# Performance work log

Measured on AMD Instinct MI355X. Metric: run time of the kernel, lower is better.

## Reference

```python
import jax, jax.numpy as jnp
import numpy as np

B, T, D = 4, 2048, 512
E, H, K = 8, 512, 2


def setup_inputs() -> dict:
    key = jax.random.key(0)
    ks = jax.random.split(key, 8)
    s_in = 1.0 / np.sqrt(D)
    s_h = 1.0 / np.sqrt(H)
    return {
        "x": jax.random.normal(ks[0], (B, T, D), dtype=jnp.float32),
        "Wg": jax.random.uniform(ks[1], (D, E), jnp.float32, -s_in, s_in),
        "bg": jax.random.uniform(ks[2], (E,), jnp.float32, -s_in, s_in),
        "W1": jax.random.uniform(ks[3], (E, D, H), jnp.float32, -s_in, s_in),
        "b1": jax.random.uniform(ks[4], (E, H), jnp.float32, -s_in, s_in),
        "W2": jax.random.uniform(ks[5], (E, H, H), jnp.float32, -s_h, s_h),
        "b2": jax.random.uniform(ks[6], (E, H), jnp.float32, -s_h, s_h),
    }


def reference(x, Wg, bg, W1, b1, W2, b2):
    Bx, Tx, Dx = x.shape
    xf = x.reshape(-1, Dx)                                   # [N, D]
    # --- gate (noise_std = 0) ---
    logits = xf @ Wg + bg                                    # [N, E]
    topk_scores, topk_idx = jax.lax.top_k(logits, K)         # [N, K]
    topk_w = jax.nn.softmax(topk_scores, axis=-1)            # K=2 -> softmax over selected
    # --- experts: dense compute, then gather the selected ones ---
    h = jax.nn.gelu(jnp.einsum('nd,edh->neh', xf, W1) + b1, approximate=False)  # [N, E, H]
    y = jnp.einsum('neh,ehf->nef', h, W2) + b2               # [N, E, H]
    sel = jnp.take_along_axis(y, topk_idx[:, :, None], axis=1)  # [N, K, H]
    out = jnp.sum(topk_w[:, :, None] * sel, axis=1)          # weighted combine [N, H]
    return out.reshape(Bx, Tx, -1)
```

## Files before the change

kernel.cpp:

```cpp
#include <hip/hip_runtime.h>
#include <hip/hip_bf16.h>


typedef __bf16 bf16x8 __attribute__((ext_vector_type(8)));
typedef float  f32x4  __attribute__((ext_vector_type(4)));

#define N_TOK 8192
#define D_IN  512
#define N_EXP 8
#define H_DIM 512

static __device__ __forceinline__ unsigned short f2bf(float f) {
    union { float f; unsigned u; } v; v.f = f;
    unsigned r = v.u + 0x7FFFu + ((v.u >> 16) & 1u);
    return (unsigned short)(r >> 16);
}
static __device__ __forceinline__ float gelu_exact(float v) {
    return 0.5f * v * (1.0f + erff(v * 0.70710678118654752f));
}
static __device__ __forceinline__ void gload_lds16(const void* src, void* lds_dst) {
    __builtin_amdgcn_global_load_lds(
        (const __attribute__((address_space(1))) unsigned int*)src,
        (__attribute__((address_space(3))) unsigned int*)lds_dst, 16, 0, 0);
}

__global__ void __launch_bounds__(256) k_pack(const float* __restrict__ W1,
                                              const float* __restrict__ W2,
                                              unsigned short* __restrict__ w1f,
                                              unsigned short* __restrict__ w2f) {
    __shared__ float t[32][65];
    int z = blockIdx.z;
    int e = z & 7;
    const float* in = (z < 8) ? W1 : W2;
    unsigned short* out = (z < 8) ? w1f : w2f;
    int cb0 = blockIdx.x * 4;
    int kc  = blockIdx.y;
    const float* src = in + ((size_t)e * 512 + kc * 32) * 512 + blockIdx.x * 64;
    int tid = threadIdx.x;
    int r = tid >> 3, cq = (tid & 7) * 8;
    float4 v0 = *(const float4*)(src + (size_t)r * 512 + cq);
    float4 v1 = *(const float4*)(src + (size_t)r * 512 + cq + 4);
    t[r][cq + 0] = v0.x; t[r][cq + 1] = v0.y; t[r][cq + 2] = v0.z; t[r][cq + 3] = v0.w;
    t[r][cq + 4] = v1.x; t[r][cq + 5] = v1.y; t[r][cq + 6] = v1.z; t[r][cq + 7] = v1.w;
    __syncthreads();
    int g = tid >> 6, lane = tid & 63;
    int l15 = lane & 15, l4 = lane >> 4;
    unsigned v[4];
    #pragma unroll
    for (int j = 0; j < 4; ++j) {
        unsigned lo = f2bf(t[l4 * 8 + 2 * j    ][g * 16 + l15]);
        unsigned hi = f2bf(t[l4 * 8 + 2 * j + 1][g * 16 + l15]);
        v[j] = lo | (hi << 16);
    }
    size_t dst = (((size_t)(e * 32 + cb0 + g) * 16 + kc) * 512) + lane * 8;
    *(uint4*)(out + dst) = make_uint4(v[0], v[1], v[2], v[3]);
}

__global__ void __launch_bounds__(256) k_gate(const float* __restrict__ x,
                                              const float* __restrict__ Wg,
                                              const float* __restrict__ bg,
                                              unsigned char* __restrict__ sel,
                                              float2* __restrict__ w2,
                                              unsigned short* __restrict__ xbf) {
    __shared__ float part[32][8][8];
    __shared__ float lg[32][8];
    int tid = threadIdx.x;
    int t = tid >> 3, c = tid & 7;
    int n0 = blockIdx.x * 32;
    int n = n0 + t;
    const float4* xr = (const float4*)(x + (size_t)n * D_IN + c * 64);
    float acc[8];
    #pragma unroll
    for (int e = 0; e < 8; ++e) acc[e] = 0.f;
    #pragma unroll
    for (int j4 = 0; j4 < 16; ++j4) {
        float4 v = xr[j4];
        int k = c * 64 + j4 * 4;
        float xv[4] = {v.x, v.y, v.z, v.w};
        #pragma unroll
        for (int u = 0; u < 4; ++u) {
            float4 wlo = *(const float4*)(Wg + (size_t)(k + u) * 8);
            float4 whi = *(const float4*)(Wg + (size_t)(k + u) * 8 + 4);
            acc[0] += xv[u] * wlo.x; acc[1] += xv[u] * wlo.y;
            acc[2] += xv[u] * wlo.z; acc[3] += xv[u] * wlo.w;
            acc[4] += xv[u] * whi.x; acc[5] += xv[u] * whi.y;
            acc[6] += xv[u] * whi.z; acc[7] += xv[u] * whi.w;
        }
    }
    #pragma unroll
    for (int e = 0; e < 8; ++e) part[t][c][e] = acc[e];
    __syncthreads();
    {
        float f = bg[c];
        #pragma unroll
        for (int cc = 0; cc < 8; ++cc) f += part[t][cc][c];
        lg[t][c] = f;
    }
    __syncthreads();
    if (c == 0) {
        float best = lg[t][0]; int i1 = 0;
        #pragma unroll
        for (int j = 1; j < 8; ++j) { float v = lg[t][j]; if (v > best) { best = v; i1 = j; } }
        float best2 = -1e30f; int i2 = 0;
        #pragma unroll
        for (int j = 0; j < 8; ++j) {
            if (j == i1) continue;
            float v = lg[t][j]; if (v > best2) { best2 = v; i2 = j; }
        }
        float tt = expf(best2 - best);
        float w0 = 1.0f / (1.0f + tt);
        sel[n] = (unsigned char)(i1 | (i2 << 4));
        w2[n] = make_float2(w0, 1.0f - w0);
    }
    #pragma unroll
    for (int i = 0; i < 8; ++i) {
        int idx = tid + i * 256;
        int r = idx >> 6, g = idx & 63;
        const float* src = x + (size_t)(n0 + r) * D_IN + g * 8;
        float4 a = *(const float4*)src;
        float4 b = *(const float4*)(src + 4);
        unsigned u0 = (unsigned)f2bf(a.x) | ((unsigned)f2bf(a.y) << 16);
        unsigned u1 = (unsigned)f2bf(a.z) | ((unsigned)f2bf(a.w) << 16);
        unsigned u2 = (unsigned)f2bf(b.x) | ((unsigned)f2bf(b.y) << 16);
        unsigned u3 = (unsigned)f2bf(b.z) | ((unsigned)f2bf(b.w) << 16);
        *(uint4*)(xbf + (size_t)(n0 + r) * D_IN + g * 8) = make_uint4(u0, u1, u2, u3);
    }
}

__global__ void __launch_bounds__(1024) k_build(const unsigned char* __restrict__ sel,
                                                const float2* __restrict__ w2,
                                                int* __restrict__ counts,
                                                int* __restrict__ lists,
                                                float* __restrict__ wgts) {
    int e = blockIdx.x;
    __shared__ int tot[8][16];
    __shared__ int cbase[8];
    int tid = threadIdx.x, lane = tid & 63, wv = tid >> 6;
    unsigned long long masks[8];
    unsigned char svals[8];
    #pragma unroll
    for (int c = 0; c < 8; ++c) {
        int n = c * 1024 + tid;
        unsigned char s = sel[n];
        svals[c] = s;
        bool f = ((s & 15) == e) || ((s >> 4) == e);
        masks[c] = __ballot(f);
        if (lane == 0) tot[c][wv] = __popcll(masks[c]);
    }
    __syncthreads();
    if (tid == 0) {
        int b = 0;
        #pragma unroll
        for (int c = 0; c < 8; ++c) {
            cbase[c] = b;
            #pragma unroll
            for (int i = 0; i < 16; ++i) b += tot[c][i];
        }
        counts[e] = b;
    }
    __syncthreads();
    #pragma unroll
    for (int c = 0; c < 8; ++c) {
        if ((masks[c] >> lane) & 1ull) {
            int wb = cbase[c];
            for (int i = 0; i < wv; ++i) wb += tot[c][i];
            int pos = wb + __popcll(masks[c] & ((1ull << lane) - 1ull));
            int n = c * 1024 + tid;
            bool f1 = ((svals[c] & 15) == e);
            lists[e * N_TOK + pos] = (n << 1) | (f1 ? 0 : 1);
            float2 w = w2[n];
            wgts[e * N_TOK + pos] = f1 ? w.x : w.y;
        }
    }
}

__global__ void __launch_bounds__(512, 4)
k_l1(const unsigned short* __restrict__ xbf,
     const unsigned short* __restrict__ w1f, const float* __restrict__ b1,
     const int* __restrict__ counts, const int* __restrict__ lists,
     unsigned short* __restrict__ hbuf) {
    __shared__ unsigned short lds[64 * D_IN];
    __shared__ int tl[64];

    int b = blockIdx.x;
    int e = b & 7;
    int rest = b >> 3;
    int tile = rest >> 1, ch = rest & 1;
    int cnt = counts[e];
    int row0 = tile * 64;
    if (row0 >= cnt) return;
    int rv = min(64, cnt - row0);
    int gb = row0;
    #pragma unroll
    for (int i = 0; i < 8; ++i) gb += (i < e) ? ((counts[i] + 63) & ~63) : 0;

    int tid = threadIdx.x, lane = tid & 63, wid = tid >> 6;
    int l15 = lane & 15, l4 = lane >> 4;
    if (tid < 64) tl[tid] = (tid < rv) ? lists[e * N_TOK + row0 + tid] : 0;

    const unsigned short* wbase = w1f + ((size_t)(e * 32 + ch * 16 + wid * 2) * 16) * 512 + (size_t)lane * 8;
    bf16x8 bb[4][2];
    #pragma unroll
    for (int n = 0; n < 2; ++n) {
        bb[0][n] = *(const bf16x8*)(wbase + (n * 16 + 0) * 512);
        bb[1][n] = *(const bf16x8*)(wbase + (n * 16 + 1) * 512);
        bb[2][n] = *(const bf16x8*)(wbase + (n * 16 + 2) * 512);
    }
    float bv[2];
    #pragma unroll
    for (int n = 0; n < 2; ++n) bv[n] = b1[e * H_DIM + ch * 256 + wid * 32 + n * 16 + l15];
    __syncthreads();

    #pragma unroll
    for (int i = 0; i < 8; ++i) {
        int row = wid * 8 + i;
        if (row < rv) {
            int tok = tl[row] >> 1;
            const char* src = (const char*)xbf + ((size_t)tok << 10)
                            + ((lane * 16) ^ ((row & 7) << 4));
            gload_lds16(src, (char*)lds + row * 1024);
        } else {
            *(uint4*)((char*)lds + row * 1024 + lane * 16) = make_uint4(0, 0, 0, 0);
        }
    }
    __syncthreads();

    f32x4 acc[4][2];
    #pragma unroll
    for (int n = 0; n < 2; ++n)
        #pragma unroll
        for (int m = 0; m < 4; ++m) acc[m][n] = f32x4{bv[n], bv[n], bv[n], bv[n]};

    #pragma unroll
    for (int kc = 0; kc < 16; ++kc) {
        if (kc + 3 < 16) {
            #pragma unroll
            for (int n = 0; n < 2; ++n)
                bb[(kc + 3) & 3][n] = *(const bf16x8*)(wbase + (n * 16 + kc + 3) * 512);
        }
        int k0 = kc * 32 + l4 * 8;
        bf16x8 a[4];
        #pragma unroll
        for (int m = 0; m < 4; ++m) {
            int row = m * 16 + l15;
            int off = (row * 1024 + k0 * 2) ^ ((row & 7) << 4);
            a[m] = *(const bf16x8*)((const char*)lds + off);
        }
        #pragma unroll
        for (int n = 0; n < 2; ++n)
            #pragma unroll
            for (int m = 0; m < 4; ++m)
                acc[m][n] = __builtin_amdgcn_mfma_f32_16x16x32_bf16(a[m], bb[kc & 3][n], acc[m][n], 0, 0, 0);
    }
    __syncthreads();

    #pragma unroll
    for (int m = 0; m < 4; ++m)
        #pragma unroll
        for (int n = 0; n < 2; ++n)
            #pragma unroll
            for (int r = 0; r < 4; ++r) {
                int row = m * 16 + l4 * 4 + r;
                int lcol = wid * 32 + n * 16 + l15;
                lds[row * 256 + lcol] = f2bf(gelu_exact(acc[m][n][r]));
            }
    __syncthreads();
    #pragma unroll
    for (int it = 0; it < 4; ++it) {
        int idx = tid + it * 512;
        int row = idx >> 5, g = idx & 31;
        if (row < rv)
            *(uint4*)(hbuf + (size_t)(gb + row) * 512 + ch * 256 + g * 8) =
                *(uint4*)(lds + row * 256 + g * 8);
    }
}

__global__ void __launch_bounds__(512, 4)
k_l2(const unsigned short* __restrict__ hbuf,
     const unsigned short* __restrict__ w2f, const float* __restrict__ b2,
     const int* __restrict__ counts, const int* __restrict__ lists,
     const float* __restrict__ wgts, float* __restrict__ out) {
    __shared__ unsigned short lds[64 * D_IN];
    __shared__ int   tl[64];
    __shared__ float wl[64];

    int b = blockIdx.x;
    int e = b & 7;
    int rest = b >> 3;
    int tile = rest >> 1, ch = rest & 1;
    int cnt = counts[e];
    int row0 = tile * 64;
    if (row0 >= cnt) return;
    int rv = min(64, cnt - row0);
    int gb = row0;
    #pragma unroll
    for (int i = 0; i < 8; ++i) gb += (i < e) ? ((counts[i] + 63) & ~63) : 0;

    int tid = threadIdx.x, lane = tid & 63, wid = tid >> 6;
    int l15 = lane & 15, l4 = lane >> 4;
    if (tid < 64) {
        int v = 0; float w = 0.f;
        if (tid < rv) {
            v = lists[e * N_TOK + row0 + tid];
            w = wgts [e * N_TOK + row0 + tid];
        }
        tl[tid] = v; wl[tid] = w;
    }

    const unsigned short* wbase = w2f + ((size_t)(e * 32 + ch * 16 + wid * 2) * 16) * 512 + (size_t)lane * 8;
    bf16x8 bb[4][2];
    #pragma unroll
    for (int n = 0; n < 2; ++n) {
        bb[0][n] = *(const bf16x8*)(wbase + (n * 16 + 0) * 512);
        bb[1][n] = *(const bf16x8*)(wbase + (n * 16 + 1) * 512);
        bb[2][n] = *(const bf16x8*)(wbase + (n * 16 + 2) * 512);
    }
    float bv[2];
    #pragma unroll
    for (int n = 0; n < 2; ++n) bv[n] = b2[e * H_DIM + ch * 256 + wid * 32 + n * 16 + l15];
    __syncthreads();

    #pragma unroll
    for (int i = 0; i < 8; ++i) {
        int row = wid * 8 + i;
        if (row < rv) {
            const char* src = (const char*)hbuf + (((size_t)(gb + row)) << 10)
                            + ((lane * 16) ^ ((row & 7) << 4));
            gload_lds16(src, (char*)lds + row * 1024);
        } else {
            *(uint4*)((char*)lds + row * 1024 + lane * 16) = make_uint4(0, 0, 0, 0);
        }
    }
    __syncthreads();

    f32x4 acc[4][2];
    #pragma unroll
    for (int n = 0; n < 2; ++n)
        #pragma unroll
        for (int m = 0; m < 4; ++m) acc[m][n] = f32x4{bv[n], bv[n], bv[n], bv[n]};

    #pragma unroll
    for (int kc = 0; kc < 16; ++kc) {
        if (kc + 3 < 16) {
            #pragma unroll
            for (int n = 0; n < 2; ++n)
                bb[(kc + 3) & 3][n] = *(const bf16x8*)(wbase + (n * 16 + kc + 3) * 512);
        }
        int k0 = kc * 32 + l4 * 8;
        bf16x8 a[4];
        #pragma unroll
        for (int m = 0; m < 4; ++m) {
            int row = m * 16 + l15;
            int off = (row * 1024 + k0 * 2) ^ ((row & 7) << 4);
            a[m] = *(const bf16x8*)((const char*)lds + off);
        }
        #pragma unroll
        for (int n = 0; n < 2; ++n)
            #pragma unroll
            for (int m = 0; m < 4; ++m)
                acc[m][n] = __builtin_amdgcn_mfma_f32_16x16x32_bf16(a[m], bb[kc & 3][n], acc[m][n], 0, 0, 0);
    }

    #pragma unroll
    for (int m = 0; m < 4; ++m)
        #pragma unroll
        for (int r = 0; r < 4; ++r) {
            int row = m * 16 + l4 * 4 + r;
            if (row < rv) {
                int t = tl[row] >> 1;
                float gw = wl[row];
                #pragma unroll
                for (int n = 0; n < 2; ++n) {
                    int col = ch * 256 + wid * 32 + n * 16 + l15;
                    atomicAdd(out + (size_t)t * H_DIM + col, gw * acc[m][n][r]);
                }
            }
        }
}

extern "C" void kernel_launch(void* const* d_in, const int* in_sizes, int n_in,
                              void* d_out, int out_size, void* d_ws, size_t ws_size,
                              hipStream_t stream) {
    (void)in_sizes; (void)n_in; (void)ws_size;
    const float* x  = (const float*)d_in[0];
    const float* Wg = (const float*)d_in[1];
    const float* bg = (const float*)d_in[2];
    const float* W1 = (const float*)d_in[3];
    const float* b1 = (const float*)d_in[4];
    const float* W2 = (const float*)d_in[5];
    const float* b2 = (const float*)d_in[6];
    float* out = (float*)d_out;

    char* ws = (char*)d_ws;
    unsigned short* w1f = (unsigned short*)(ws);
    unsigned short* w2f = (unsigned short*)(ws + (4ull << 20));
    unsigned short* hbuf= (unsigned short*)(ws + (8ull << 20));
    unsigned short* xbf = (unsigned short*)(ws + (25ull << 20));
    char* tail = ws + (33ull << 20);
    int*   counts = (int*)(tail);
    int*   lists  = (int*)(tail + 256);
    float* wgts   = (float*)(tail + 256 + 262144);
    unsigned char* sel = (unsigned char*)(tail + 256 + 524288);
    float2* w2g   = (float2*)(tail + 256 + 532480);

    hipMemsetAsync(out, 0, (size_t)out_size * sizeof(float), stream);

    k_pack<<<dim3(8, 16, 16), dim3(256), 0, stream>>>(W1, W2, w1f, w2f);
    k_gate<<<dim3(N_TOK / 32), dim3(256), 0, stream>>>(x, Wg, bg, sel, w2g, xbf);
    k_build<<<dim3(N_EXP), dim3(1024), 0, stream>>>(sel, w2g, counts, lists, wgts);
    k_l1<<<dim3(2048), dim3(512), 0, stream>>>(xbf, w1f, b1, counts, lists, hbuf);
    k_l2<<<dim3(2048), dim3(512), 0, stream>>>(hbuf, w2f, b2, counts, lists, wgts, out);
}
```

Baseline: 181.8 us.

## Replace atomic scatter-add combine with bf16 slot buffer and separate combine kernel

The second-layer kernel no longer atomically adds weighted results into the output. It stages each gate-weighted tile in LDS as bf16 and writes it with coalesced stores into a per-(token, slot) buffer. A new combine kernel sums the two slots per token into fp32 output, which also removes the output memset. This trades scattered fp32 atomics for an extra kernel launch and round trip through memory, and it rounds each expert's contribution to bf16 before the sum.

```diff
diff --git a/kernel.cpp b/kernel.cpp
--- a/kernel.cpp
+++ b/kernel.cpp
@@ -14,6 +14,9 @@
     union { float f; unsigned u; } v; v.f = f;
     unsigned r = v.u + 0x7FFFu + ((v.u >> 16) & 1u);
     return (unsigned short)(r >> 16);
+}
+static __device__ __forceinline__ float bf2f(unsigned short h) {
+    union { unsigned u; float f; } v; v.u = ((unsigned)h) << 16; return v.f;
 }
 static __device__ __forceinline__ float gelu_exact(float v) {
     return 0.5f * v * (1.0f + erff(v * 0.70710678118654752f));
@@ -279,7 +282,8 @@
 k_l2(const unsigned short* __restrict__ hbuf,
      const unsigned short* __restrict__ w2f, const float* __restrict__ b2,
      const int* __restrict__ counts, const int* __restrict__ lists,
-     const float* __restrict__ wgts, float* __restrict__ out) {
+     const float* __restrict__ wgts,
+     unsigned short* __restrict__ ybuf) {
     __shared__ unsigned short lds[64 * D_IN];
     __shared__ int   tl[64];
     __shared__ float wl[64];
@@ -361,27 +365,52 @@
                 acc[m][n] = __builtin_amdgcn_mfma_f32_16x16x32_bf16(a[m], bb[kc & 3][n], acc[m][n], 0, 0, 0);
     }
 
+    __syncthreads();
     #pragma unroll
     for (int m = 0; m < 4; ++m)
         #pragma unroll
-        for (int r = 0; r < 4; ++r) {
-            int row = m * 16 + l4 * 4 + r;
-            if (row < rv) {
-                int t = tl[row] >> 1;
-                float gw = wl[row];
-                #pragma unroll
-                for (int n = 0; n < 2; ++n) {
-                    int col = ch * 256 + wid * 32 + n * 16 + l15;
-                    atomicAdd(out + (size_t)t * H_DIM + col, gw * acc[m][n][r]);
-                }
+        for (int n = 0; n < 2; ++n)
+            #pragma unroll
+            for (int r = 0; r < 4; ++r) {
+                int row = m * 16 + l4 * 4 + r;
+                int lcol = wid * 32 + n * 16 + l15;
+                lds[row * 256 + lcol] = f2bf(acc[m][n][r] * wl[row]);
             }
-        }
+    __syncthreads();
+    #pragma unroll
+    for (int it = 0; it < 4; ++it) {
+        int idx = tid + it * 512;
+        int row = idx >> 5, g = idx & 31;
+        if (row < rv)
+            *(uint4*)(ybuf + (size_t)tl[row] * 512 + ch * 256 + g * 8) =
+                *(uint4*)(lds + row * 256 + g * 8);
+    }
+}
+
+__global__ void __launch_bounds__(256) k_combine(const unsigned short* __restrict__ yb,
+                                                 float* __restrict__ out) {
+    int gid = blockIdx.x * 256 + threadIdx.x;
+    int n = gid >> 6;
+    int h0 = (gid & 63) * 8;
+    const unsigned short* r0 = yb + ((size_t)2 * n) * H_DIM + h0;
+    uint4 a = *(const uint4*)r0;
+    uint4 b = *(const uint4*)(r0 + H_DIM);
+    float o[8];
+    unsigned ua[4] = {a.x, a.y, a.z, a.w}, ub[4] = {b.x, b.y, b.z, b.w};
+    #pragma unroll
+    for (int j = 0; j < 4; ++j) {
+        o[2 * j]     = bf2f((unsigned short)(ua[j] & 0xFFFF)) + bf2f((unsigned short)(ub[j] & 0xFFFF));
+        o[2 * j + 1] = bf2f((unsigned short)(ua[j] >> 16))    + bf2f((unsigned short)(ub[j] >> 16));
+    }
+    float* dst = out + (size_t)n * H_DIM + h0;
+    *(float4*)dst       = make_float4(o[0], o[1], o[2], o[3]);
+    *(float4*)(dst + 4) = make_float4(o[4], o[5], o[6], o[7]);
 }
 
 extern "C" void kernel_launch(void* const* d_in, const int* in_sizes, int n_in,
                               void* d_out, int out_size, void* d_ws, size_t ws_size,
                               hipStream_t stream) {
-    (void)in_sizes; (void)n_in; (void)ws_size;
+    (void)in_sizes; (void)n_in; (void)ws_size; (void)out_size;
     const float* x  = (const float*)d_in[0];
     const float* Wg = (const float*)d_in[1];
     const float* bg = (const float*)d_in[2];
@@ -394,20 +423,20 @@
     char* ws = (char*)d_ws;
     unsigned short* w1f = (unsigned short*)(ws);
     unsigned short* w2f = (unsigned short*)(ws + (4ull << 20));
-    unsigned short* hbuf= (unsigned short*)(ws + (8ull << 20));
-    unsigned short* xbf = (unsigned short*)(ws + (25ull << 20));
-    char* tail = ws + (33ull << 20);
+    unsigned short* ybuf= (unsigned short*)(ws + (8ull << 20));
+    unsigned short* hbuf= (unsigned short*)(ws + (24ull << 20));
+    unsigned short* xbf = (unsigned short*)(ws + (41ull << 20));
+    char* tail = ws + (49ull << 20);
     int*   counts = (int*)(tail);
     int*   lists  = (int*)(tail + 256);
     float* wgts   = (float*)(tail + 256 + 262144);
     unsigned char* sel = (unsigned char*)(tail + 256 + 524288);
     float2* w2g   = (float2*)(tail + 256 + 532480);
 
-    hipMemsetAsync(out, 0, (size_t)out_size * sizeof(float), stream);
-
     k_pack<<<dim3(8, 16, 16), dim3(256), 0, stream>>>(W1, W2, w1f, w2f);
     k_gate<<<dim3(N_TOK / 32), dim3(256), 0, stream>>>(x, Wg, bg, sel, w2g, xbf);
     k_build<<<dim3(N_EXP), dim3(1024), 0, stream>>>(sel, w2g, counts, lists, wgts);
     k_l1<<<dim3(2048), dim3(512), 0, stream>>>(xbf, w1f, b1, counts, lists, hbuf);
-    k_l2<<<dim3(2048), dim3(512), 0, stream>>>(hbuf, w2f, b2, counts, lists, wgts, out);
-}
+    k_l2<<<dim3(2048), dim3(512), 0, stream>>>(hbuf, w2f, b2, counts, lists, wgts, ybuf);
+    k_combine<<<dim3(N_TOK * 64 / 256), dim3(256), 0, stream>>>(ybuf, out);
+}
```

Measured after the change: 166.6 us. 8.4% less time.
